# Optimization experiments

Measured on AMD Instinct MI355X. Metric: run time of the kernel, lower is better.

## Reference

```python
import jax, jax.numpy as jnp
import numpy as np

N_NODES = 100000
N_EDGES = 1600000
IN_FEATS = 128
N_HIDDEN = 128
N_CLASSES = 64


def setup_inputs() -> dict:
    key = jax.random.key(0)
    ks = jax.random.split(key, 8)
    def glorot(k, shape):
        fan_in, fan_out = shape
        lim = (6.0 / (fan_in + fan_out)) ** 0.5
        return jax.random.uniform(k, shape, jnp.float32, -lim, lim)
    return {
        "x": jax.random.normal(ks[0], (N_NODES, IN_FEATS), jnp.float32),
        "W_self1": glorot(ks[1], (IN_FEATS, N_HIDDEN)),
        "W_neigh1": glorot(ks[2], (IN_FEATS, N_HIDDEN)),
        "b1": jnp.zeros((N_HIDDEN,), jnp.float32),
        "W_self2": glorot(ks[3], (N_HIDDEN, N_HIDDEN)),
        "W_neigh2": glorot(ks[4], (N_HIDDEN, N_HIDDEN)),
        "b2": jnp.zeros((N_HIDDEN,), jnp.float32),
        "W_out": glorot(ks[5], (N_HIDDEN, N_CLASSES)),
        "b_out": jnp.zeros((N_CLASSES,), jnp.float32),
        "edge_src": jax.random.randint(ks[6], (N_EDGES,), 0, N_NODES, jnp.int32),
        "edge_dst": jax.random.randint(ks[7], (N_EDGES,), 0, N_NODES, jnp.int32),
    }


def reference(x, W_self1, W_neigh1, b1, W_self2, W_neigh2, b2, W_out, b_out,
              edge_src, edge_dst):
    n = x.shape[0]
    # in-degree for mean aggregation (clamped to 1 to avoid div-by-zero)
    deg = jax.ops.segment_sum(jnp.ones_like(edge_dst, jnp.float32), edge_dst,
                              num_segments=n)
    inv_deg = 1.0 / jnp.maximum(deg, 1.0)  # [N]

    def sage_conv(h, W_self, W_neigh, b):
        # mean aggregation: gather src features, scatter-sum to dst, divide by degree
        msg_sum = jax.ops.segment_sum(h[edge_src], edge_dst, num_segments=n)
        h_neigh = msg_sum * inv_deg[:, None]            # [N, d]
        return h @ W_self + h_neigh @ W_neigh + b       # fc_self + fc_neigh + bias

    # layer 0 + relu (dropout is identity in eval mode)
    h = jax.nn.relu(sage_conv(x, W_self1, W_neigh1, b1))
    # layer 1 + relu
    h = jax.nn.relu(sage_conv(h, W_self2, W_neigh2, b2))
    # final linear classifier
    return h @ W_out + b_out
```

## Files before the change

### kernel.cpp

```cpp
#include <hip/hip_runtime.h>
#include <hip/hip_bf16.h>


#define N_FEATS 128
#define CAP 64
#define TILE 4096

typedef __attribute__((ext_vector_type(8))) short bf16x8;
typedef __attribute__((ext_vector_type(4))) float f32x4;

__device__ __forceinline__ ushort f2b(float f) {
    union { float f; unsigned u; } c; c.f = f;
    unsigned u = c.u + 0x7fffu + ((c.u >> 16) & 1u);
    return (ushort)(u >> 16);
}
__device__ __forceinline__ float b2f(ushort b) {
    union { unsigned u; float f; } c; c.u = ((unsigned)b) << 16;
    return c.f;
}

__global__ __launch_bounds__(256) void k_hist(const int* __restrict__ dst,
                                              int* __restrict__ bucketCnt, int E) {
    __shared__ int h[512];
    int t = threadIdx.x;
    h[t] = 0; h[t + 256] = 0;
    __syncthreads();
    int base0 = blockIdx.x * TILE;
#pragma unroll
    for (int j = 0; j < 16; ++j) {
        int i = base0 + j * 256 + t;
        if (i < E) atomicAdd(&h[dst[i] >> 8], 1);
    }
    __syncthreads();
    for (int b = t; b < 512; b += 256)
        if (h[b] > 0) atomicAdd(&bucketCnt[b], h[b]);
}

__global__ void k_bscan(const int* __restrict__ bucketCnt, int* __restrict__ base,
                        int* __restrict__ cursor, int NB, int E) {
    __shared__ int s[512];
    int t = threadIdx.x;
    int v = (t < NB) ? bucketCnt[t] : 0;
    s[t] = v;
    __syncthreads();
    for (int off = 1; off < 512; off <<= 1) {
        int x = 0;
        if (t >= off) x = s[t - off];
        __syncthreads();
        if (t >= off) s[t] += x;
        __syncthreads();
    }
    if (t < NB) { int b = s[t] - v; base[t] = b; cursor[t] = b; }
    if (t == 0) base[NB] = E;
}

__global__ __launch_bounds__(256) void k_scatter(const int* __restrict__ src,
                                                 const int* __restrict__ dst,
                                                 int* __restrict__ cursor,
                                                 int* __restrict__ ebuf, int E) {
    __shared__ int th[512];
    int t = threadIdx.x;
    th[t] = 0; th[t + 256] = 0;
    __syncthreads();
    int base0 = blockIdx.x * TILE;
    int pk[16], bk[16], rk[16];
#pragma unroll
    for (int j = 0; j < 16; ++j) {
        int i = base0 + j * 256 + t;
        bk[j] = -1;
        if (i < E) {
            int d = dst[i], s = src[i];
            bk[j] = d >> 8;
            pk[j] = ((d & 255) << 17) | s;
            rk[j] = atomicAdd(&th[bk[j]], 1);
        }
    }
    __syncthreads();
    for (int b = t; b < 512; b += 256) {
        int c = th[b];
        if (c > 0) th[b] = atomicAdd(&cursor[b], c);
    }
    __syncthreads();
#pragma unroll
    for (int j = 0; j < 16; ++j)
        if (bk[j] >= 0) ebuf[th[bk[j]] + rk[j]] = pk[j];
}

__global__ __launch_bounds__(256) void k_csr(const int* __restrict__ base,
                                             const int* __restrict__ ebuf,
                                             int* __restrict__ cnt,
                                             int* __restrict__ colF, int N) {
    __shared__ int cl[256];
    int t = threadIdx.x, b = blockIdx.x;
    cl[t] = 0;
    __syncthreads();
    int lo = base[b], hi = base[b + 1];
    int node0 = b << 8;
    for (int i = lo + t; i < hi; i += 256) {
        int p = ebuf[i];
        int s = p & 0x1FFFF;
        int dl = p >> 17;
        int r = atomicAdd(&cl[dl], 1);
        if (r < CAP) colF[((size_t)(node0 + dl)) * CAP + r] = s;
    }
    __syncthreads();
    int n = node0 + t;
    if (n < N) cnt[n] = cl[t];
}

__global__ void k_prep(const float* __restrict__ x, ushort* __restrict__ xb, int n4,
                       const float* __restrict__ Ws1, const float* __restrict__ Wn1,
                       const float* __restrict__ Ws2, const float* __restrict__ Wn2,
                       const float* __restrict__ Wo,
                       ushort* __restrict__ o1, ushort* __restrict__ o2,
                       ushort* __restrict__ o3, ushort* __restrict__ o4,
                       ushort* __restrict__ o5, ushort* __restrict__ hzrow, int N) {
    int i = blockIdx.x * blockDim.x + threadIdx.x;
    if (i < n4) {
        float4 v = ((const float4*)x)[i];
        ushort4 o;
        o.x = f2b(v.x); o.y = f2b(v.y); o.z = f2b(v.z); o.w = f2b(v.w);
        ((ushort4*)xb)[i] = o;
    } else {
        int q = i - n4;
        if (q < 65536) {
            int w = q >> 14, j = q & 16383;
            const float* W = (w == 0) ? Ws1 : (w == 1) ? Wn1 : (w == 2) ? Ws2 : Wn2;
            ushort* O = (w == 0) ? o1 : (w == 1) ? o2 : (w == 2) ? o3 : o4;
            int k = j >> 7, n = j & 127;
            O[n * 128 + k] = f2b(W[j]);
        } else if (q < 65536 + 8192) {
            int j = q - 65536;
            int k = j >> 6, n = j & 63;
            o5[n * 128 + k] = f2b(Wo[j]);
        } else if (q < 65536 + 8192 + 64) {
            int j = q - (65536 + 8192);
            ushort4 z = {0, 0, 0, 0};
            if (j < 32) ((ushort4*)&xb[(size_t)N * N_FEATS])[j] = z;
            else        ((ushort4*)hzrow)[j - 32] = z;
        }
    }
}

__global__ __launch_bounds__(256) void k_agg(const ushort* __restrict__ h,
                                             const int* __restrict__ cnt,
                                             const int* __restrict__ colF,
                                             ushort* __restrict__ hn, int N) {
    int n = blockIdx.x * 4 + (threadIdx.x >> 6);
    if (n >= N) return;
    int lane = threadIdx.x & 63;
    int g = lane >> 4;
    int f = lane & 15;
    int degT = cnt[n];
    int deg = degT > CAP ? CAP : degT;
    const int* __restrict__ row = &colF[(size_t)n * CAP];
    float acc[8];
#pragma unroll
    for (int k = 0; k < 8; ++k) acc[k] = 0.f;

    for (int j0 = 0; j0 < deg; j0 += 16) {
        int last = deg - 1;
        int ja = j0 + g, jb = j0 + 4 + g, jc = j0 + 8 + g, jd = j0 + 12 + g;
        int sa = __builtin_nontemporal_load(&row[min(ja, last)]);
        int sb = __builtin_nontemporal_load(&row[min(jb, last)]);
        int sc = __builtin_nontemporal_load(&row[min(jc, last)]);
        int sd = __builtin_nontemporal_load(&row[min(jd, last)]);
        sa = (ja < deg) ? sa : N;
        sb = (jb < deg) ? sb : N;
        sc = (jc < deg) ? sc : N;
        sd = (jd < deg) ? sd : N;
        bf16x8 va = *(const bf16x8*)&h[(size_t)sa * N_FEATS + f * 8];
        bf16x8 vb = *(const bf16x8*)&h[(size_t)sb * N_FEATS + f * 8];
        bf16x8 vc = *(const bf16x8*)&h[(size_t)sc * N_FEATS + f * 8];
        bf16x8 vd = *(const bf16x8*)&h[(size_t)sd * N_FEATS + f * 8];
#pragma unroll
        for (int k = 0; k < 8; ++k) {
            acc[k] += b2f((ushort)va[k]);
            acc[k] += b2f((ushort)vb[k]);
            acc[k] += b2f((ushort)vc[k]);
            acc[k] += b2f((ushort)vd[k]);
        }
    }
#pragma unroll
    for (int k = 0; k < 8; ++k) {
        acc[k] += __shfl_xor(acc[k], 16, 64);
        acc[k] += __shfl_xor(acc[k], 32, 64);
    }
    if (g == 0) {
        float inv = 1.f / fmaxf((float)degT, 1.f);
        bf16x8 o;
#pragma unroll
        for (int k = 0; k < 8; ++k) o[k] = (short)f2b(acc[k] * inv);
        *(bf16x8*)&hn[(size_t)n * N_FEATS + f * 8] = o;
    }
}

__global__ __launch_bounds__(256) void k_mm1(const ushort* __restrict__ A1,
                                             const ushort* __restrict__ Wst,
                                             const ushort* __restrict__ HN,
                                             const ushort* __restrict__ Wnt,
                                             const float* __restrict__ bias,
                                             ushort* __restrict__ Hout, int M) {
    constexpr int LDA = 40;
    __shared__ ushort As[128 * LDA];
    __shared__ ushort Bs[128 * LDA];
    const int t = threadIdx.x;
    const int w = t >> 6, lane = t & 63;
    const int l15 = lane & 15, quad = lane >> 4;
    const int wr = (w >> 1) * 64, wc = (w & 1) * 64;
    const int row0 = blockIdx.x * 128;

    f32x4 acc[4][4];
#pragma unroll
    for (int mi = 0; mi < 4; ++mi)
#pragma unroll
        for (int ni = 0; ni < 4; ++ni) acc[mi][ni] = (f32x4){0.f, 0.f, 0.f, 0.f};

    for (int kt = 0; kt < 8; ++kt) {
        const ushort* __restrict__ A = (kt < 4) ? A1 : HN;
        const ushort* __restrict__ W = (kt < 4) ? Wst : Wnt;
        const int k0 = (kt & 3) * 32;
        __syncthreads();
#pragma unroll
        for (int i = 0; i < 2; ++i) {
            int slot = t + i * 256;
            int r = slot >> 2, ko = (slot & 3) * 8;
            int row = row0 + r;
            if (row >= M) row = M - 1;
            *(bf16x8*)&As[r * LDA + ko] = *(const bf16x8*)&A[(size_t)row * N_FEATS + k0 + ko];
            *(bf16x8*)&Bs[r * LDA + ko] = *(const bf16x8*)&W[(size_t)r * N_FEATS + k0 + ko];
        }
        __syncthreads();
        bf16x8 af[4];
#pragma unroll
        for (int mi = 0; mi < 4; ++mi)
            af[mi] = *(const bf16x8*)&As[(wr + mi * 16 + l15) * LDA + quad * 8];
#pragma unroll
        for (int ni = 0; ni < 4; ++ni) {
            bf16x8 bfr = *(const bf16x8*)&Bs[(wc + ni * 16 + l15) * LDA + quad * 8];
#pragma unroll
            for (int mi = 0; mi < 4; ++mi)
                acc[mi][ni] = __builtin_amdgcn_mfma_f32_16x16x32_bf16(
                    af[mi], bfr, acc[mi][ni], 0, 0, 0);
        }
    }
#pragma unroll
    for (int ni = 0; ni < 4; ++ni) {
        int c = wc + ni * 16 + l15;
        float bv = bias[c];
#pragma unroll
        for (int mi = 0; mi < 4; ++mi)
#pragma unroll
            for (int r = 0; r < 4; ++r) {
                int row = row0 + wr + mi * 16 + quad * 4 + r;
                if (row < M)
                    Hout[(size_t)row * N_FEATS + c] = f2b(fmaxf(acc[mi][ni][r] + bv, 0.f));
            }
    }
}

__global__ __launch_bounds__(256) void k_mm2cls(const ushort* __restrict__ A1,
                                                const ushort* __restrict__ Wst,
                                                const ushort* __restrict__ HN,
                                                const ushort* __restrict__ Wnt,
                                                const float* __restrict__ bias,
                                                const ushort* __restrict__ Wot,
                                                const float* __restrict__ bout,
                                                float* __restrict__ OutF, int M) {
    constexpr int LDA = 40;
    __shared__ ushort As[128 * LDA];
    __shared__ ushort Bs[128 * LDA];
    const int t = threadIdx.x;
    const int w = t >> 6, lane = t & 63;
    const int l15 = lane & 15, quad = lane >> 4;
    const int wr = (w >> 1) * 64, wc = (w & 1) * 64;
    const int row0 = blockIdx.x * 128;

    f32x4 acc[4][4];
#pragma unroll
    for (int mi = 0; mi < 4; ++mi)
#pragma unroll
        for (int ni = 0; ni < 4; ++ni) acc[mi][ni] = (f32x4){0.f, 0.f, 0.f, 0.f};

    for (int kt = 0; kt < 8; ++kt) {
        const ushort* __restrict__ A = (kt < 4) ? A1 : HN;
        const ushort* __restrict__ W = (kt < 4) ? Wst : Wnt;
        const int k0 = (kt & 3) * 32;
        __syncthreads();
#pragma unroll
        for (int i = 0; i < 2; ++i) {
            int slot = t + i * 256;
            int r = slot >> 2, ko = (slot & 3) * 8;
            int row = row0 + r;
            if (row >= M) row = M - 1;
            *(bf16x8*)&As[r * LDA + ko] = *(const bf16x8*)&A[(size_t)row * N_FEATS + k0 + ko];
            *(bf16x8*)&Bs[r * LDA + ko] = *(const bf16x8*)&W[(size_t)r * N_FEATS + k0 + ko];
        }
        __syncthreads();
        bf16x8 af[4];
#pragma unroll
        for (int mi = 0; mi < 4; ++mi)
            af[mi] = *(const bf16x8*)&As[(wr + mi * 16 + l15) * LDA + quad * 8];
#pragma unroll
        for (int ni = 0; ni < 4; ++ni) {
            bf16x8 bfr = *(const bf16x8*)&Bs[(wc + ni * 16 + l15) * LDA + quad * 8];
#pragma unroll
            for (int mi = 0; mi < 4; ++mi)
                acc[mi][ni] = __builtin_amdgcn_mfma_f32_16x16x32_bf16(
                    af[mi], bfr, acc[mi][ni], 0, 0, 0);
        }
    }

    f32x4 acc2[2][4];
#pragma unroll
    for (int mi = 0; mi < 2; ++mi)
#pragma unroll
        for (int ni = 0; ni < 4; ++ni) acc2[mi][ni] = (f32x4){0.f, 0.f, 0.f, 0.f};

    for (int kt = 0; kt < 4; ++kt) {
        const int k0 = kt * 32;
        __syncthreads();
        {
            int r = t >> 2, ko = (t & 3) * 8;
            if (r < 64)
                *(bf16x8*)&Bs[r * LDA + ko] =
                    *(const bf16x8*)&Wot[(size_t)r * N_FEATS + k0 + ko];
        }
        if ((w & 1) == (k0 >> 6)) {
            int ni0 = (k0 & 63) >> 4;
#pragma unroll
            for (int d = 0; d < 2; ++d) {
                int ni = ni0 + d;
                int c = wc + ni * 16 + l15;
                int cc = c - k0;
                float bv = bias[c];
#pragma unroll
                for (int mi = 0; mi < 4; ++mi)
#pragma unroll
                    for (int r = 0; r < 4; ++r) {
                        int lrow = wr + mi * 16 + quad * 4 + r;
                        As[lrow * LDA + cc] = f2b(fmaxf(acc[mi][ni][r] + bv, 0.f));
                    }
            }
        }
        __syncthreads();
        bf16x8 af2[2];
#pragma unroll
        for (int mi = 0; mi < 2; ++mi)
            af2[mi] = *(const bf16x8*)&As[(w * 32 + mi * 16 + l15) * LDA + quad * 8];
#pragma unroll
        for (int ni = 0; ni < 4; ++ni) {
            bf16x8 bfr = *(const bf16x8*)&Bs[(ni * 16 + l15) * LDA + quad * 8];
#pragma unroll
            for (int mi = 0; mi < 2; ++mi)
                acc2[mi][ni] = __builtin_amdgcn_mfma_f32_16x16x32_bf16(
                    af2[mi], bfr, acc2[mi][ni], 0, 0, 0);
        }
    }
#pragma unroll
    for (int ni = 0; ni < 4; ++ni) {
        int c = ni * 16 + l15;
        float bv = bout[c];
#pragma unroll
        for (int mi = 0; mi < 2; ++mi)
#pragma unroll
            for (int r = 0; r < 4; ++r) {
                int row = row0 + w * 32 + mi * 16 + quad * 4 + r;
                if (row < M)
                    OutF[(size_t)row * 64 + c] = acc2[mi][ni][r] + bv;
            }
    }
}

extern "C" void kernel_launch(void* const* d_in, const int* in_sizes, int n_in,
                              void* d_out, int out_size, void* d_ws, size_t ws_size,
                              hipStream_t stream) {
    const float* x        = (const float*)d_in[0];
    const float* W_self1  = (const float*)d_in[1];
    const float* W_neigh1 = (const float*)d_in[2];
    const float* b1       = (const float*)d_in[3];
    const float* W_self2  = (const float*)d_in[4];
    const float* W_neigh2 = (const float*)d_in[5];
    const float* b2       = (const float*)d_in[6];
    const float* W_out    = (const float*)d_in[7];
    const float* b_out    = (const float*)d_in[8];
    const int* edge_src   = (const int*)d_in[9];
    const int* edge_dst   = (const int*)d_in[10];

    const int N = in_sizes[0] / N_FEATS;
    const int E = in_sizes[9];
    float* out = (float*)d_out;

    char* ws = (char*)d_ws;
    size_t o = 0;
    auto carve = [&](size_t bytes) -> char* {
        char* p = ws + o;
        o += (bytes + 255) & ~(size_t)255;
        return p;
    };
    ushort* xb    = (ushort*)carve((size_t)(N + 1) * N_FEATS * 2);
    ushort* h     = (ushort*)carve((size_t)(N + 1) * N_FEATS * 2);
    ushort* hn    = (ushort*)carve((size_t)N * N_FEATS * 2);
    int* colF     = (int*)carve((size_t)N * CAP * 4);
    int* cnt      = (int*)carve((size_t)N * 4);
    int* ebuf     = (int*)carve((size_t)E * 4);
    int* bucketCnt= (int*)carve(512 * 4);
    int* bbase    = (int*)carve(513 * 4);
    int* bcursor  = (int*)carve(512 * 4);
    ushort* Ws1t  = (ushort*)carve(128 * 128 * 2);
    ushort* Wn1t  = (ushort*)carve(128 * 128 * 2);
    ushort* Ws2t  = (ushort*)carve(128 * 128 * 2);
    ushort* Wn2t  = (ushort*)carve(128 * 128 * 2);
    ushort* Wot   = (ushort*)carve(64 * 128 * 2);
    (void)ws_size;

    const int NB = (N + 255) >> 8;
    const int NT = (E + TILE - 1) / TILE;
    const int n4 = N * N_FEATS / 4;

    hipMemsetAsync(bucketCnt, 0, 512 * 4, stream);
    k_hist<<<NT, 256, 0, stream>>>(edge_dst, bucketCnt, E);
    k_bscan<<<1, 512, 0, stream>>>(bucketCnt, bbase, bcursor, NB, E);
    k_scatter<<<NT, 256, 0, stream>>>(edge_src, edge_dst, bcursor, ebuf, E);
    k_csr<<<NB, 256, 0, stream>>>(bbase, ebuf, cnt, colF, N);
    k_prep<<<(n4 + 65536 + 8192 + 64 + 255) / 256, 256, 0, stream>>>(
        x, xb, n4, W_self1, W_neigh1, W_self2, W_neigh2, W_out,
        Ws1t, Wn1t, Ws2t, Wn2t, Wot, &h[(size_t)N * N_FEATS], N);

    const int GB = (N + 127) / 128;
    const int AB = (N + 3) / 4;

    k_agg<<<AB, 256, 0, stream>>>(xb, cnt, colF, hn, N);
    k_mm1<<<GB, 256, 0, stream>>>(xb, Ws1t, hn, Wn1t, b1, h, N);
    k_agg<<<AB, 256, 0, stream>>>(h, cnt, colF, hn, N);
    k_mm2cls<<<GB, 256, 0, stream>>>(h, Ws2t, hn, Wn2t, b2, Wot, b_out, out, N);
}
```

Baseline: 348.7 us.

## Fuse histogram with prep, drop bucket-scan kernel, pack bf16 unpacking in aggregation

The histogram kernel is merged with the bf16 conversion/weight-transpose prep into one launch. The single-block bucket scan kernel is removed; each scatter and CSR block now recomputes the 512-entry prefix scan redundantly in shared memory from the bucket counts. The aggregation kernel unpacks bf16 pairs from 32-bit words with shift/mask into float2 accumulators to allow packed adds. This cuts two launches and a serial scan step at the cost of redundant per-block scan work.

```diff
diff --git a/kernel.cpp b/kernel.cpp
--- a/kernel.cpp
+++ b/kernel.cpp
@@ -8,57 +8,102 @@
 
 typedef __attribute__((ext_vector_type(8))) short bf16x8;
 typedef __attribute__((ext_vector_type(4))) float f32x4;
+typedef __attribute__((ext_vector_type(2))) float f32x2;
 
 __device__ __forceinline__ ushort f2b(float f) {
     union { float f; unsigned u; } c; c.f = f;
     unsigned u = c.u + 0x7fffu + ((c.u >> 16) & 1u);
     return (ushort)(u >> 16);
 }
-__device__ __forceinline__ float b2f(ushort b) {
-    union { unsigned u; float f; } c; c.u = ((unsigned)b) << 16;
+__device__ __forceinline__ float u2f(unsigned u) {
+    union { unsigned u; float f; } c; c.u = u;
     return c.f;
 }
 
-__global__ __launch_bounds__(256) void k_hist(const int* __restrict__ dst,
-                                              int* __restrict__ bucketCnt, int E) {
+__device__ __forceinline__ void scan512(const int* __restrict__ gsrc,
+                                        int* sA, int* sB, int t) {
+    sA[t] = gsrc[t];
+    sA[t + 256] = gsrc[t + 256];
+    __syncthreads();
+    int* src = sA;
+    int* dst = sB;
+    for (int off = 1; off < 512; off <<= 1) {
+#pragma unroll
+        for (int i = t; i < 512; i += 256) {
+            int v = src[i];
+            if (i >= off) v += src[i - off];
+            dst[i] = v;
+        }
+        __syncthreads();
+        int* tmp = src; src = dst; dst = tmp;
+    }
+    if (src != sA) {
+        sA[t] = src[t];
+        sA[t + 256] = src[t + 256];
+        __syncthreads();
+    }
+}
+
+__global__ __launch_bounds__(256) void k_histprep(
+    const int* __restrict__ dst, int* __restrict__ bucketCnt, int E, int NT,
+    const float* __restrict__ x, ushort* __restrict__ xb, int n4,
+    const float* __restrict__ Ws1, const float* __restrict__ Wn1,
+    const float* __restrict__ Ws2, const float* __restrict__ Wn2,
+    const float* __restrict__ Wo,
+    ushort* __restrict__ o1, ushort* __restrict__ o2,
+    ushort* __restrict__ o3, ushort* __restrict__ o4,
+    ushort* __restrict__ o5, ushort* __restrict__ hzrow, int N) {
     __shared__ int h[512];
     int t = threadIdx.x;
-    h[t] = 0; h[t + 256] = 0;
-    __syncthreads();
-    int base0 = blockIdx.x * TILE;
-#pragma unroll
-    for (int j = 0; j < 16; ++j) {
-        int i = base0 + j * 256 + t;
-        if (i < E) atomicAdd(&h[dst[i] >> 8], 1);
-    }
-    __syncthreads();
-    for (int b = t; b < 512; b += 256)
-        if (h[b] > 0) atomicAdd(&bucketCnt[b], h[b]);
-}
-
-__global__ void k_bscan(const int* __restrict__ bucketCnt, int* __restrict__ base,
-                        int* __restrict__ cursor, int NB, int E) {
-    __shared__ int s[512];
-    int t = threadIdx.x;
-    int v = (t < NB) ? bucketCnt[t] : 0;
-    s[t] = v;
-    __syncthreads();
-    for (int off = 1; off < 512; off <<= 1) {
-        int x = 0;
-        if (t >= off) x = s[t - off];
-        __syncthreads();
-        if (t >= off) s[t] += x;
-        __syncthreads();
-    }
-    if (t < NB) { int b = s[t] - v; base[t] = b; cursor[t] = b; }
-    if (t == 0) base[NB] = E;
+    if (blockIdx.x < NT) {
+        h[t] = 0; h[t + 256] = 0;
+        __syncthreads();
+        int base0 = blockIdx.x * TILE;
+#pragma unroll
+        for (int j = 0; j < 16; ++j) {
+            int i = base0 + j * 256 + t;
+            if (i < E) atomicAdd(&h[dst[i] >> 8], 1);
+        }
+        __syncthreads();
+        for (int b = t; b < 512; b += 256)
+            if (h[b] > 0) atomicAdd(&bucketCnt[b], h[b]);
+    } else {
+        int i = (blockIdx.x - NT) * 256 + t;
+        if (i < n4) {
+            float4 v = ((const float4*)x)[i];
+            ushort4 o;
+            o.x = f2b(v.x); o.y = f2b(v.y); o.z = f2b(v.z); o.w = f2b(v.w);
+            ((ushort4*)xb)[i] = o;
+        } else {
+            int q = i - n4;
+            if (q < 65536) {
+                int w = q >> 14, j = q & 16383;
+                const float* W = (w == 0) ? Ws1 : (w == 1) ? Wn1 : (w == 2) ? Ws2 : Wn2;
+                ushort* O = (w == 0) ? o1 : (w == 1) ? o2 : (w == 2) ? o3 : o4;
+                int k = j >> 7, n = j & 127;
+                O[n * 128 + k] = f2b(W[j]);
+            } else if (q < 65536 + 8192) {
+                int j = q - 65536;
+                int k = j >> 6, n = j & 63;
+                o5[n * 128 + k] = f2b(Wo[j]);
+            } else if (q < 65536 + 8192 + 64) {
+                int j = q - (65536 + 8192);
+                ushort4 z = {0, 0, 0, 0};
+                if (j < 32) ((ushort4*)&xb[(size_t)N * N_FEATS])[j] = z;
+                else        ((ushort4*)hzrow)[j - 32] = z;
+            }
+        }
+    }
 }
 
 __global__ __launch_bounds__(256) void k_scatter(const int* __restrict__ src,
                                                  const int* __restrict__ dst,
-                                                 int* __restrict__ cursor,
+                                                 const int* __restrict__ bucketCnt,
+                                                 int* __restrict__ cursor0,
                                                  int* __restrict__ ebuf, int E) {
     __shared__ int th[512];
+    __shared__ int sA[512];
+    __shared__ int sB[512];
     int t = threadIdx.x;
     th[t] = 0; th[t + 256] = 0;
     __syncthreads();
@@ -76,9 +121,13 @@
         }
     }
     __syncthreads();
+    scan512(bucketCnt, sA, sB, t);
     for (int b = t; b < 512; b += 256) {
         int c = th[b];
-        if (c > 0) th[b] = atomicAdd(&cursor[b], c);
+        if (c > 0) {
+            int base_b = sA[b] - bucketCnt[b];
+            th[b] = base_b + atomicAdd(&cursor0[b], c);
+        }
     }
     __syncthreads();
 #pragma unroll
@@ -86,15 +135,19 @@
         if (bk[j] >= 0) ebuf[th[bk[j]] + rk[j]] = pk[j];
 }
 
-__global__ __launch_bounds__(256) void k_csr(const int* __restrict__ base,
+__global__ __launch_bounds__(256) void k_csr(const int* __restrict__ bucketCnt,
                                              const int* __restrict__ ebuf,
                                              int* __restrict__ cnt,
                                              int* __restrict__ colF, int N) {
     __shared__ int cl[256];
+    __shared__ int sA[512];
+    __shared__ int sB[512];
     int t = threadIdx.x, b = blockIdx.x;
     cl[t] = 0;
     __syncthreads();
-    int lo = base[b], hi = base[b + 1];
+    scan512(bucketCnt, sA, sB, t);
+    int hi = sA[b];
+    int lo = hi - bucketCnt[b];
     int node0 = b << 8;
     for (int i = lo + t; i < hi; i += 256) {
         int p = ebuf[i];
@@ -106,40 +159,6 @@
     __syncthreads();
     int n = node0 + t;
     if (n < N) cnt[n] = cl[t];
-}
-
-__global__ void k_prep(const float* __restrict__ x, ushort* __restrict__ xb, int n4,
-                       const float* __restrict__ Ws1, const float* __restrict__ Wn1,
-                       const float* __restrict__ Ws2, const float* __restrict__ Wn2,
-                       const float* __restrict__ Wo,
-                       ushort* __restrict__ o1, ushort* __restrict__ o2,
-                       ushort* __restrict__ o3, ushort* __restrict__ o4,
-                       ushort* __restrict__ o5, ushort* __restrict__ hzrow, int N) {
-    int i = blockIdx.x * blockDim.x + threadIdx.x;
-    if (i < n4) {
-        float4 v = ((const float4*)x)[i];
-        ushort4 o;
-        o.x = f2b(v.x); o.y = f2b(v.y); o.z = f2b(v.z); o.w = f2b(v.w);
-        ((ushort4*)xb)[i] = o;
-    } else {
-        int q = i - n4;
-        if (q < 65536) {
-            int w = q >> 14, j = q & 16383;
-            const float* W = (w == 0) ? Ws1 : (w == 1) ? Wn1 : (w == 2) ? Ws2 : Wn2;
-            ushort* O = (w == 0) ? o1 : (w == 1) ? o2 : (w == 2) ? o3 : o4;
-            int k = j >> 7, n = j & 127;
-            O[n * 128 + k] = f2b(W[j]);
-        } else if (q < 65536 + 8192) {
-            int j = q - 65536;
-            int k = j >> 6, n = j & 63;
-            o5[n * 128 + k] = f2b(Wo[j]);
-        } else if (q < 65536 + 8192 + 64) {
-            int j = q - (65536 + 8192);
-            ushort4 z = {0, 0, 0, 0};
-            if (j < 32) ((ushort4*)&xb[(size_t)N * N_FEATS])[j] = z;
-            else        ((ushort4*)hzrow)[j - 32] = z;
-        }
-    }
 }
 
 __global__ __launch_bounds__(256) void k_agg(const ushort* __restrict__ h,
@@ -154,9 +173,9 @@
     int degT = cnt[n];
     int deg = degT > CAP ? CAP : degT;
     const int* __restrict__ row = &colF[(size_t)n * CAP];
-    float acc[8];
-#pragma unroll
-    for (int k = 0; k < 8; ++k) acc[k] = 0.f;
+    f32x2 acc[4];
+#pragma unroll
+    for (int k = 0; k < 4; ++k) acc[k] = (f32x2){0.f, 0.f};
 
     for (int j0 = 0; j0 < deg; j0 += 16) {
         int last = deg - 1;
@@ -169,29 +188,41 @@
         sb = (jb < deg) ? sb : N;
         sc = (jc < deg) ? sc : N;
         sd = (jd < deg) ? sd : N;
-        bf16x8 va = *(const bf16x8*)&h[(size_t)sa * N_FEATS + f * 8];
-        bf16x8 vb = *(const bf16x8*)&h[(size_t)sb * N_FEATS + f * 8];
-        bf16x8 vc = *(const bf16x8*)&h[(size_t)sc * N_FEATS + f * 8];
-        bf16x8 vd = *(const bf16x8*)&h[(size_t)sd * N_FEATS + f * 8];
-#pragma unroll
-        for (int k = 0; k < 8; ++k) {
-            acc[k] += b2f((ushort)va[k]);
-            acc[k] += b2f((ushort)vb[k]);
-            acc[k] += b2f((ushort)vc[k]);
-            acc[k] += b2f((ushort)vd[k]);
-        }
-    }
-#pragma unroll
-    for (int k = 0; k < 8; ++k) {
-        acc[k] += __shfl_xor(acc[k], 16, 64);
-        acc[k] += __shfl_xor(acc[k], 32, 64);
+        uint4 va = *(const uint4*)&h[(size_t)sa * N_FEATS + f * 8];
+        uint4 vb = *(const uint4*)&h[(size_t)sb * N_FEATS + f * 8];
+        uint4 vc = *(const uint4*)&h[(size_t)sc * N_FEATS + f * 8];
+        uint4 vd = *(const uint4*)&h[(size_t)sd * N_FEATS + f * 8];
+        unsigned wa[4] = {va.x, va.y, va.z, va.w};
+        unsigned wb[4] = {vb.x, vb.y, vb.z, vb.w};
+        unsigned wc[4] = {vc.x, vc.y, vc.z, vc.w};
+        unsigned wd[4] = {vd.x, vd.y, vd.z, vd.w};
+#pragma unroll
+        for (int k = 0; k < 4; ++k) {
+            acc[k] += (f32x2){u2f(wa[k] << 16), u2f(wa[k] & 0xffff0000u)};
+            acc[k] += (f32x2){u2f(wb[k] << 16), u2f(wb[k] & 0xffff0000u)};
+            acc[k] += (f32x2){u2f(wc[k] << 16), u2f(wc[k] & 0xffff0000u)};
+            acc[k] += (f32x2){u2f(wd[k] << 16), u2f(wd[k] & 0xffff0000u)};
+        }
+    }
+#pragma unroll
+    for (int k = 0; k < 4; ++k) {
+        acc[k].x += __shfl_xor(acc[k].x, 16, 64);
+        acc[k].y += __shfl_xor(acc[k].y, 16, 64);
+        acc[k].x += __shfl_xor(acc[k].x, 32, 64);
+        acc[k].y += __shfl_xor(acc[k].y, 32, 64);
     }
     if (g == 0) {
         float inv = 1.f / fmaxf((float)degT, 1.f);
-        bf16x8 o;
-#pragma unroll
-        for (int k = 0; k < 8; ++k) o[k] = (short)f2b(acc[k] * inv);
-        *(bf16x8*)&hn[(size_t)n * N_FEATS + f * 8] = o;
+        uint4 o;
+        unsigned ow[4];
+#pragma unroll
+        for (int k = 0; k < 4; ++k) {
+            unsigned lo = f2b(acc[k].x * inv);
+            unsigned hi = f2b(acc[k].y * inv);
+            ow[k] = lo | (hi << 16);
+        }
+        o.x = ow[0]; o.y = ow[1]; o.z = ow[2]; o.w = ow[3];
+        *(uint4*)&hn[(size_t)n * N_FEATS + f * 8] = o;
     }
 }
 
@@ -404,28 +435,29 @@
     int* colF     = (int*)carve((size_t)N * CAP * 4);
     int* cnt      = (int*)carve((size_t)N * 4);
     int* ebuf     = (int*)carve((size_t)E * 4);
-    int* bucketCnt= (int*)carve(512 * 4);
-    int* bbase    = (int*)carve(513 * 4);
-    int* bcursor  = (int*)carve(512 * 4);
+    int* bwork    = (int*)carve(1024 * 4);
     ushort* Ws1t  = (ushort*)carve(128 * 128 * 2);
     ushort* Wn1t  = (ushort*)carve(128 * 128 * 2);
     ushort* Ws2t  = (ushort*)carve(128 * 128 * 2);
     ushort* Wn2t  = (ushort*)carve(128 * 128 * 2);
     ushort* Wot   = (ushort*)carve(64 * 128 * 2);
     (void)ws_size;
+    int* bucketCnt = bwork;
+    int* cursor0   = bwork + 512;
 
     const int NB = (N + 255) >> 8;
     const int NT = (E + TILE - 1) / TILE;
     const int n4 = N * N_FEATS / 4;
-
-    hipMemsetAsync(bucketCnt, 0, 512 * 4, stream);
-    k_hist<<<NT, 256, 0, stream>>>(edge_dst, bucketCnt, E);
-    k_bscan<<<1, 512, 0, stream>>>(bucketCnt, bbase, bcursor, NB, E);
-    k_scatter<<<NT, 256, 0, stream>>>(edge_src, edge_dst, bcursor, ebuf, E);
-    k_csr<<<NB, 256, 0, stream>>>(bbase, ebuf, cnt, colF, N);
-    k_prep<<<(n4 + 65536 + 8192 + 64 + 255) / 256, 256, 0, stream>>>(
+    const int PREP = n4 + 65536 + 8192 + 64;
+    const int PREP_B = (PREP + 255) / 256;
+
+    hipMemsetAsync(bwork, 0, 1024 * 4, stream);
+    k_histprep<<<NT + PREP_B, 256, 0, stream>>>(
+        edge_dst, bucketCnt, E, NT,
         x, xb, n4, W_self1, W_neigh1, W_self2, W_neigh2, W_out,
         Ws1t, Wn1t, Ws2t, Wn2t, Wot, &h[(size_t)N * N_FEATS], N);
+    k_scatter<<<NT, 256, 0, stream>>>(edge_src, edge_dst, bucketCnt, cursor0, ebuf, E);
+    k_csr<<<NB, 256, 0, stream>>>(bucketCnt, ebuf, cnt, colF, N);
 
     const int GB = (N + 127) / 128;
     const int AB = (N + 3) / 4;
```

New measurement: 341.6 us. 1.02x faster.
